# Kernel tuning notes

Hardware: AMD Instinct MI355X
Metric: run time of the kernel (lower is better)

Reference implementation:

```python
import jax, jax.numpy as jnp
from jax import lax
import numpy as np

SLOPE = 0.01   # torch nn.LeakyReLU default
EPS = 1e-5     # BN eps
DN = ('NCDHW', 'OIDHW', 'NCDHW')


def conv3d(x, w, pad):
    return lax.conv_general_dilated(x, w, (1, 1, 1), pad, dimension_numbers=DN)


def bn(x, g, b):
    # BatchNorm1d over all active points == per-channel stats over (N, D, H, W)
    m = jnp.mean(x, axis=(0, 2, 3, 4), keepdims=True)
    v = jnp.var(x, axis=(0, 2, 3, 4), keepdims=True)
    return (x - m) * lax.rsqrt(v + EPS) * g.reshape(1, -1, 1, 1, 1) + b.reshape(1, -1, 1, 1, 1)


def lrelu(x):
    return jnp.where(x >= 0, x, SLOPE * x)


def setup_inputs() -> dict:
    key = jax.random.key(0)
    ks = jax.random.split(key, 8)
    Cin, Cout = 128, 64
    x = jax.random.normal(ks[0], (1, Cin, 16, 48, 48), jnp.float32)      # coarse sparse grid (all-active)
    skip = jax.random.normal(ks[1], (1, Cout, 32, 96, 96), jnp.float32)  # fine skip grid
    s = lambda k, shape, fan: jax.random.normal(k, shape, jnp.float32) * np.float32(1.0 / np.sqrt(fan))
    w_trans = s(ks[2], (Cout, Cin, 3, 3, 3), Cin * 27)
    w_up = s(ks[3], (Cout, Cout, 3, 3, 3), Cout * 27)
    w1 = s(ks[4], (Cout, Cout, 1, 3, 3), Cout * 9)
    w2 = s(ks[5], (Cout, Cout, 3, 1, 3), Cout * 9)
    w3 = s(ks[6], (Cout, Cout, 3, 3, 3), Cout * 27)
    g = jnp.ones((Cout,), jnp.float32)
    b = jnp.zeros((Cout,), jnp.float32)
    return dict(x=x, skip=skip, w_trans=w_trans, g_t=g, b_t=b, w_up=w_up,
                w1=w1, g1=g, b1=b, w2=w2, g2=g, b2=b, w3=w3, g3=g, b3=b)


def reference(x, skip, w_trans, g_t, b_t, w_up, w1, g1, b1, w2, g2, b2, w3, g3, b3):
    # trans_conv (subm 3x3x3) -> LeakyReLU -> BN
    xt = bn(lrelu(conv3d(x, w_trans, [(1, 1)] * 3)), g_t, b_t)
    up = lax.conv_general_dilated(xt, w_up, (1, 1, 1), [(1, 2)] * 3,
                                  lhs_dilation=(2, 2, 2), dimension_numbers=DN)
    up = up + skip
    up = bn(lrelu(conv3d(up, w1, [(0, 0), (1, 1), (1, 1)])), g1, b1)  # conv1x3 (1,3,3)
    up = bn(lrelu(conv3d(up, w2, [(1, 1), (0, 0), (1, 1)])), g2, b2)  # conv3x1 (3,1,3)
    up = bn(lrelu(conv3d(up, w3, [(1, 1)] * 3)), g3, b3)              # conv3x3 (3,3,3)
    return up
```

## Files before the change

kernel.cpp:

```cpp
#include <hip/hip_runtime.h>

#define SLOPE 0.01f
#define BN_EPS 1e-5f

typedef __attribute__((ext_vector_type(8))) short short8;
typedef __attribute__((ext_vector_type(4))) float f32x4;

static constexpr int D1 = 32, H1 = 96, W1_ = 96;
static constexpr int HW1 = H1 * W1_, DHW1 = D1 * HW1;
static constexpr int D0 = 16, H0 = 48, W0 = 48;
static constexpr int HW0 = H0 * W0, DHW0 = D0 * HW0;

static constexpr int FP_PLPTS = 98 * 98;
static constexpr int CP_PLPTS = 50 * 50;
static constexpr int FP_ELEMS = 33 * FP_PLPTS * 64;

__device__ __forceinline__ short f2bf(float f) {
    unsigned u = __builtin_bit_cast(unsigned, f);
    unsigned r = (u + 0x7fffu + ((u >> 16) & 1u)) >> 16;
    return (short)r;
}
__device__ __forceinline__ float bf2f(short s) {
    unsigned u = ((unsigned)(unsigned short)s) << 16;
    return __builtin_bit_cast(float, u);
}
__device__ __forceinline__ int pidx_fine(int s) {
    int z = s / HW1; int r = s - z * HW1; int y = r / W1_; int x = r - y * W1_;
    return z * FP_PLPTS + (y + 1) * 98 + (x + 1);
}
__device__ __forceinline__ int pidx_coarse(int s) {
    int z = s / HW0; int r = s - z * HW0; int y = r / W0; int x = r - y * W0;
    return z * CP_PLPTS + (y + 1) * 50 + (x + 1);
}
__device__ __forceinline__ void gload16(const void* g, void* l) {
    __builtin_amdgcn_global_load_lds(
        (const __attribute__((address_space(1))) void*)g,
        (__attribute__((address_space(3))) void*)l, 16, 0, 0);
}

__global__ __launch_bounds__(256)
void to_cl_pad128(const float* __restrict__ in, short* __restrict__ out)
{
    __shared__ float t[64][65];
    const int s0 = blockIdx.x * 64, c0 = blockIdx.y * 64;
    const int tid = threadIdx.x;
    {
        const int cpr = tid >> 2, ch = tid & 3;
        const float4* ip = (const float4*)(in + (size_t)(c0 + cpr) * DHW0 + s0 + ch * 16);
        #pragma unroll
        for (int i = 0; i < 4; ++i) {
            float4 v = ip[i]; int sb = ch * 16 + i * 4;
            t[sb][cpr] = v.x; t[sb + 1][cpr] = v.y; t[sb + 2][cpr] = v.z; t[sb + 3][cpr] = v.w;
        }
    }
    __syncthreads();
    {
        const int spr = tid >> 2, cc = (tid & 3) * 16;
        short8 o0, o1;
        #pragma unroll
        for (int q = 0; q < 8; ++q) { o0[q] = f2bf(t[spr][cc + q]); o1[q] = f2bf(t[spr][cc + 8 + q]); }
        const int p = pidx_coarse(s0 + spr);
        short* op = out + (size_t)p * 128 + c0 + cc;
        *(short8*)op = o0;
        *(short8*)(op + 8) = o1;
    }
}

__global__ __launch_bounds__(256)
void to_cl_bf16(const float* __restrict__ in, short* __restrict__ out, int S)
{
    __shared__ float t[64][65];
    const int s0 = blockIdx.x * 64;
    const int tid = threadIdx.x;
    {
        const int cpr = tid >> 2, ch = tid & 3;
        const float4* ip = (const float4*)(in + (size_t)cpr * S + s0 + ch * 16);
        #pragma unroll
        for (int i = 0; i < 4; ++i) {
            float4 v = ip[i]; int sb = ch * 16 + i * 4;
            t[sb][cpr] = v.x; t[sb + 1][cpr] = v.y; t[sb + 2][cpr] = v.z; t[sb + 3][cpr] = v.w;
        }
    }
    __syncthreads();
    {
        const int spr = tid >> 2, cc = (tid & 3) * 16;
        short8 o0, o1;
        #pragma unroll
        for (int q = 0; q < 8; ++q) { o0[q] = f2bf(t[spr][cc + q]); o1[q] = f2bf(t[spr][cc + 8 + q]); }
        short* op = out + (size_t)(s0 + spr) * 64 + cc;
        *(short8*)op = o0;
        *(short8*)(op + 8) = o1;
    }
}

__device__ __forceinline__ void rp(const float* __restrict__ w, short* __restrict__ dst,
                                   int CIN, int KSZ, int i)
{
    int t = i / (64 * CIN); int r = i % (64 * CIN); int o = r / CIN; int ci = r % CIN;
    dst[i] = f2bf(w[(size_t)(o * CIN + ci) * KSZ + t]);
}
__global__ __launch_bounds__(256)
void prep_all(const float* __restrict__ wt, const float* __restrict__ wu,
              const float* __restrict__ w1, const float* __restrict__ w2,
              const float* __restrict__ w3, short* dt, short* du,
              short* d1, short* d2, short* d3)
{
    int i = blockIdx.x * 256 + threadIdx.x;
    if (i < 221184) { rp(wt, dt, 128, 27, i); return; } i -= 221184;
    if (i < 110592) { rp(wu, du, 64, 27, i); return; } i -= 110592;
    if (i < 36864)  { rp(w1, d1, 64, 9, i);  return; } i -= 36864;
    if (i < 36864)  { rp(w2, d2, 64, 9, i);  return; } i -= 36864;
    if (i < 110592) rp(w3, d3, 64, 27, i);
}

__global__ void finalize_stats(const float* __restrict__ stats, const float* __restrict__ g,
                               const float* __restrict__ b, float invN, float* __restrict__ aff)
{
    int c = threadIdx.x;
    float m = stats[c] * invN;
    float var = stats[64 + c] * invN - m * m;
    float rstd = rsqrtf(var + BN_EPS);
    float sc = g[c] * rstd;
    aff[c] = sc;
    aff[64 + c] = b[c] - m * sc;
}

template<int MODE>
__global__ __launch_bounds__(256)
void affine_pad(short* __restrict__ buf, const float* __restrict__ aff, int n8)
{
    int i = blockIdx.x * 256 + threadIdx.x;
    if (i >= n8) return;
    int s = i >> 3, cb = (i & 7) * 8;
    int p = (MODE == 1) ? pidx_fine(s) : pidx_coarse(s);
    short* ptr = buf + (size_t)p * 64 + cb;
    short8 v = *(const short8*)ptr;
    short8 o;
    #pragma unroll
    for (int q = 0; q < 8; ++q) {
        int c = cb + q;
        o[q] = f2bf(bf2f(v[q]) * aff[c] + aff[64 + c]);
    }
    *(short8*)ptr = o;
}

__global__ __launch_bounds__(256)
void final_out(const short* __restrict__ in, float* __restrict__ out, const float* __restrict__ aff)
{
    __shared__ float t[64][65];
    const int s0 = blockIdx.x * 64;
    const int tid = threadIdx.x;
    {
        const int spr = tid >> 2, ch = tid & 3;
        const short8* ip = (const short8*)(in + (size_t)(s0 + spr) * 64 + ch * 16);
        short8 v0 = ip[0], v1 = ip[1];
        #pragma unroll
        for (int q = 0; q < 8; ++q) { int c = ch * 16 + q;     t[spr][c] = bf2f(v0[q]) * aff[c] + aff[64 + c]; }
        #pragma unroll
        for (int q = 0; q < 8; ++q) { int c = ch * 16 + 8 + q; t[spr][c] = bf2f(v1[q]) * aff[c] + aff[64 + c]; }
    }
    __syncthreads();
    {
        const int c = tid >> 2, sc = (tid & 3) * 16;
        #pragma unroll
        for (int i = 0; i < 4; ++i) {
            float4 w;
            w.x = t[sc + 4 * i][c]; w.y = t[sc + 4 * i + 1][c];
            w.z = t[sc + 4 * i + 2][c]; w.w = t[sc + 4 * i + 3][c];
            *(float4*)(out + (size_t)c * DHW1 + s0 + sc + 4 * i) = w;
        }
    }
}

__global__ __launch_bounds__(256)
void zero_misc(short* __restrict__ PadA, short* __restrict__ PadB,
               short* __restrict__ X0, short* __restrict__ Y0, float* __restrict__ stats)
{
    const short8 z8 = {0, 0, 0, 0, 0, 0, 0, 0};
    int i = blockIdx.x * 256 + threadIdx.x;
    constexpr int T_F = 33 * 3104 + 76832;
    constexpr int T_X = 17 * 3136 + 40000;
    constexpr int T_Y = 17 * 1568 + 20000;
    constexpr int TOT = 2 * T_F + T_X + T_Y + 128;
    if (i >= TOT) return;

    auto fine_off = [](int q) -> size_t {
        if (q < 33 * 3104) {
            int pl = q / 3104, e = q % 3104, p = e >> 3, c = e & 7;
            int y, x;
            if (p < 98) { y = 0; x = p; }
            else if (p < 196) { y = 97; x = p - 98; }
            else { int q2 = p - 196; y = 1 + (q2 >> 1); x = (q2 & 1) ? 97 : 0; }
            return ((size_t)pl * FP_PLPTS + y * 98 + x) * 64 + c * 8;
        }
        int q2 = q - 33 * 3104;
        return (size_t)32 * FP_PLPTS * 64 + (size_t)q2 * 8;
    };
    auto co_off = [](int q, int CPR) -> size_t {
        const int EPP = 196 * CPR;
        if (q < 17 * EPP) {
            int pl = q / EPP, e = q % EPP, p = e / CPR, c = e % CPR;
            int y, x;
            if (p < 50) { y = 0; x = p; }
            else if (p < 100) { y = 49; x = p - 50; }
            else { int r = p - 100; y = 1 + (r >> 1); x = (r & 1) ? 49 : 0; }
            return ((size_t)pl * CP_PLPTS + y * 50 + x) * (CPR * 8) + c * 8;
        }
        int q2 = q - 17 * EPP;
        return (size_t)16 * CP_PLPTS * (CPR * 8) + (size_t)q2 * 8;
    };

    if (i < T_F) { *(short8*)(PadA + fine_off(i)) = z8; return; } i -= T_F;
    if (i < T_F) { *(short8*)(PadB + fine_off(i)) = z8; return; } i -= T_F;
    if (i < T_X) { *(short8*)(X0 + co_off(i, 16)) = z8; return; } i -= T_X;
    if (i < T_Y) { *(short8*)(Y0 + co_off(i, 8)) = z8; return; } i -= T_Y;
    float4 zf = {0.f, 0.f, 0.f, 0.f};
    *(float4*)((char*)stats + (size_t)i * 16) = zf;
}

template<int MG, int CIN, int KD, int KH, int KW, int PD, int PH, int PW,
         int GD, int GH, int GW, int OUTMODE, bool STATS>
__global__ __launch_bounds__(256, 2)
void convmm5(const short* __restrict__ A, const short* __restrict__ Wt,
             short* __restrict__ Out, float* __restrict__ stats)
{
    constexpr int MR   = 64 * MG;
    constexpr int KSZ  = KD * KH * KW;
    constexpr int PPW  = GW + 2;
    constexpr int PLP  = (GH + 2) * PPW;
    constexpr int HWg  = GH * GW;
    constexpr int CPR  = CIN / 8;
    constexpr int L2C  = (CIN == 64) ? 3 : 4;
    constexpr int RPI  = 64 / CPR;
    constexpr int ASZ  = MR * CIN * 2;
    constexpr int BSZ  = 64 * CIN * 2;
    constexpr int API  = ASZ / 4096;
    constexpr int BPI  = BSZ / 4096;
    constexpr int KCN  = CIN / 32;
    constexpr int S_IF = API + BPI;

    __shared__ char smem[2 * ASZ + 2 * BSZ];

    const int tid = threadIdx.x, lane = tid & 63, wave = tid >> 6;
    const int rl = lane & 15, kg = lane >> 4;

    const int nwg = gridDim.x;
    const int bid = blockIdx.x;
    const int bswz = (nwg & 7) ? bid : ((bid & 7) * (nwg >> 3) + (bid >> 3));
    const int row0 = bswz * MR;

    int zA[API], yxA[API], cofA[API];
    #pragma unroll
    for (int i = 0; i < API; ++i) {
        const int gi = wave * API + i;
        const int r = gi * RPI + (lane >> L2C);
        const int s = row0 + r;
        const int z = s / HWg; const int rm = s - z * HWg;
        const int y = rm / GW; const int x = rm - y * GW;
        zA[i] = z;
        yxA[i] = (y + 1) * PPW + (x + 1);
        cofA[i] = ((lane & (CPR - 1)) ^ (r & 7)) * 8;
    }
    int rB[BPI], cofB[BPI];
    #pragma unroll
    for (int i = 0; i < BPI; ++i) {
        const int gi = wave * BPI + i;
        const int r = gi * RPI + (lane >> L2C);
        rB[i] = r;
        cofB[i] = ((lane & (CPR - 1)) ^ (r & 7)) * 8;
    }

    auto stageA = [&](int bsel, int kd, int kh, int kw) {
        const int dyx = (kh - PH) * PPW + (kw - PW);
        #pragma unroll
        for (int i = 0; i < API; ++i) {
            int zp = zA[i] + (kd - PD);
            int pl = ((unsigned)zp < (unsigned)GD) ? zp : GD;
            const short* src = A + ((size_t)pl * PLP + yxA[i] + dyx) * CIN + cofA[i];
            void* dst = smem + bsel * ASZ + (wave * API + i) * 1024;
            gload16(src, dst);
        }
    };
    auto stageB = [&](int bsel, int t) {
        const short* wt = Wt + (size_t)t * 64 * CIN;
        #pragma unroll
        for (int i = 0; i < BPI; ++i) {
            const short* src = wt + rB[i] * CIN + cofB[i];
            void* dst = smem + 2 * ASZ + bsel * BSZ + (wave * BPI + i) * 1024;
            gload16(src, dst);
        }
    };

    f32x4 acc[MG][4];
    #pragma unroll
    for (int mg = 0; mg < MG; ++mg)
        #pragma unroll
        for (int ng = 0; ng < 4; ++ng)
            acc[mg][ng] = (f32x4){0.f, 0.f, 0.f, 0.f};

    auto comp = [&](int bsel) {
        const short* ab = (const short*)(smem + bsel * ASZ);
        const short* bb = (const short*)(smem + 2 * ASZ + bsel * BSZ);
        #pragma unroll
        for (int kc = 0; kc < KCN; ++kc) {
            short8 av[MG], bv[4];
            #pragma unroll
            for (int mg = 0; mg < MG; ++mg) {
                const int r = wave * (16 * MG) + mg * 16 + rl;
                const int c = (kc * 4 + kg) ^ (r & 7);
                av[mg] = *(const short8*)(ab + r * CIN + c * 8);
            }
            #pragma unroll
            for (int ng = 0; ng < 4; ++ng) {
                const int r = ng * 16 + rl;
                const int c = (kc * 4 + kg) ^ (r & 7);
                bv[ng] = *(const short8*)(bb + r * CIN + c * 8);
            }
            __builtin_amdgcn_s_setprio(1);
            #pragma unroll
            for (int mg = 0; mg < MG; ++mg)
                #pragma unroll
                for (int ng = 0; ng < 4; ++ng)
                    acc[mg][ng] = __builtin_amdgcn_mfma_f32_16x16x32_bf16(av[mg], bv[ng], acc[mg][ng], 0, 0, 0);
            __builtin_amdgcn_s_setprio(0);
        }
    };

    stageA(0, 0, 0, 0);
    stageB(0, 0);

    #pragma unroll
    for (int t = 0; t < KSZ; ++t) {
        const int cur = t & 1;
        if (t + 1 < KSZ) {
            const int t1 = t + 1;
            const int kd = t1 / (KH * KW), rm = t1 % (KH * KW);
            stageA(cur ^ 1, kd, rm / KW, rm % KW);
            stageB(cur ^ 1, t1);
            asm volatile("s_waitcnt vmcnt(%0)" :: "i"(S_IF) : "memory");
        } else {
            asm volatile("s_waitcnt vmcnt(0)" ::: "memory");
        }
        __builtin_amdgcn_s_barrier();
        __builtin_amdgcn_sched_barrier(0);
        comp(cur);
        asm volatile("s_waitcnt lgkmcnt(0)" ::: "memory");
        __builtin_amdgcn_sched_barrier(0);
        __builtin_amdgcn_s_barrier();
    }

    short (*tile)[64] = (short(*)[64])smem;
    float* red = (float*)(smem + 2 * ASZ);

    #pragma unroll
    for (int mg = 0; mg < MG; ++mg)
        #pragma unroll
        for (int ng = 0; ng < 4; ++ng)
            #pragma unroll
            for (int j = 0; j < 4; ++j) {
                float v = acc[mg][ng][j];
                if (STATS) v = (v >= 0.f) ? v : SLOPE * v;
                tile[wave * (16 * MG) + mg * 16 + kg * 4 + j][ng * 16 + rl] = f2bf(v);
            }
    __syncthreads();

    #pragma unroll
    for (int i = 0; i < MR / 32; ++i) {
        const int chunk = i * 256 + tid;
        const int r = chunk >> 3, cc = (chunk & 7) * 8;
        const int s = row0 + r;
        size_t o;
        if (OUTMODE == 0)      o = (size_t)s * 64 + cc;
        else if (OUTMODE == 1) o = (size_t)pidx_fine(s) * 64 + cc;
        else                   o = (size_t)pidx_coarse(s) * 64 + cc;
        *(short8*)(Out + o) = *(const short8*)&tile[r][cc];
    }

    if (STATS) {
        float s1 = 0.f, s2 = 0.f;
        const int col = tid & 63, rg = tid >> 6;
        #pragma unroll 4
        for (int r = rg * (MR / 4); r < (rg + 1) * (MR / 4); ++r) {
            float v = bf2f(tile[r][col]); s1 += v; s2 += v * v;
        }
        red[rg * 64 + col] = s1;
        red[256 + rg * 64 + col] = s2;
        __syncthreads();
        if (tid < 64) {
            float a = red[tid] + red[64 + tid] + red[128 + tid] + red[192 + tid];
            float b = red[256 + tid] + red[320 + tid] + red[384 + tid] + red[448 + tid];
            atomicAdd(&stats[tid], a);
            atomicAdd(&stats[64 + tid], b);
        }
    }
}

template<int KD, int KH, int PD, int PH, int OUTMODE, bool STATS>
__global__ __launch_bounds__(128, 1)
void convmm7(const short* __restrict__ A, const short* __restrict__ Wt,
             short* __restrict__ Out, float* __restrict__ stats)
{
    constexpr int KSZ = KD * KH * 3, NG = KD * KH;
    constexpr int PLP = FP_PLPTS;
    constexpr int ABYTES = 208 * 128;
    constexpr int BBYTES = 8192;
    __shared__ __align__(16) char smem[2 * ABYTES + 2 * BBYTES];

    const int tid = threadIdx.x, lane = tid & 63, wave = tid >> 6;
    const int rl = lane & 15, kg = lane >> 4;

    const int nwg = gridDim.x, bid = blockIdx.x;
    const int bswz = (bid & 7) * (nwg >> 3) + (bid >> 3);
    const int s0 = bswz * 192;
    const int z0 = s0 / HW1;
    const int y0 = (s0 - z0 * HW1) / 96;

    const int ptl = lane >> 3;
    const int csl = (lane & 7) ^ ptl;

    auto stageA = [&](int bsel, int g) {
        const int kd = g / KH, kh = g % KH;
        const int zp = z0 + kd - PD;
        const int pl = ((unsigned)zp < 32u) ? zp : 32;
        const int ys = y0 + kh - PH;
        const size_t base = (size_t)pl * PLP + (size_t)(ys + 1) * 98;
        #pragma unroll
        for (int i = 0; i < 13; ++i) {
            const int ii = wave * 13 + i;
            const short* src = A + (base + ii * 8 + ptl) * 64 + csl * 8;
            gload16(src, smem + bsel * ABYTES + ii * 1024);
        }
    };
    auto stageB = [&](int bsel, int t) {
        const short* wt = Wt + (size_t)t * 4096;
        #pragma unroll
        for (int i = 0; i < 4; ++i) {
            const int ii = wave * 4 + i;
            const short* src = wt + (ii * 8 + ptl) * 64 + csl * 8;
            gload16(src, smem + 2 * ABYTES + bsel * BBYTES + ii * 1024);
        }
    };

    f32x4 acc[6][4];
    #pragma unroll
    for (int mg = 0; mg < 6; ++mg)
        #pragma unroll
        for (int ng = 0; ng < 4; ++ng)
            acc[mg][ng] = (f32x4){0.f, 0.f, 0.f, 0.f};

    const int jb = wave * 98 + rl;

    stageA(0, 0);
    stageB(0, 0);

    #pragma unroll
    for (int t = 0; t < KSZ; ++t) {
        const int g = t / 3, kw = t % 3;
        if (kw == 0 && g + 1 < NG) stageA((g + 1) & 1, g + 1);
        if (t + 1 < KSZ) stageB((t + 1) & 1, t + 1);
        if (t == KSZ - 1)
            asm volatile("s_waitcnt vmcnt(0)" ::: "memory");
        else if (kw == 0 && g + 1 < NG)
            asm volatile("s_waitcnt vmcnt(17)" ::: "memory");
        else
            asm volatile("s_waitcnt vmcnt(4)" ::: "memory");
        __builtin_amdgcn_s_barrier();
        __builtin_amdgcn_sched_barrier(0);

        const char* ab = smem + (g & 1) * ABYTES;
        const char* bb = smem + 2 * ABYTES + (t & 1) * BBYTES;
        #pragma unroll
        for (int kc = 0; kc < 2; ++kc) {
            short8 bv[4], av[6];
            #pragma unroll
            for (int ng = 0; ng < 4; ++ng) {
                const int row = ng * 16 + rl;
                bv[ng] = *(const short8*)(bb + row * 128 + (((kc * 4 + kg) ^ (rl & 7)) << 4));
            }
            #pragma unroll
            for (int mg = 0; mg < 6; ++mg) {
                const int j = jb + mg * 16 + kw;
                av[mg] = *(const short8*)(ab + j * 128 + (((kc * 4 + kg) ^ (j & 7)) << 4));
            }
            __builtin_amdgcn_s_setprio(1);
            #pragma unroll
            for (int mg = 0; mg < 6; ++mg)
                #pragma unroll
                for (int ng = 0; ng < 4; ++ng)
                    acc[mg][ng] = __builtin_amdgcn_mfma_f32_16x16x32_bf16(av[mg], bv[ng], acc[mg][ng], 0, 0, 0);
            __builtin_amdgcn_s_setprio(0);
        }
        asm volatile("s_waitcnt lgkmcnt(0)" ::: "memory");
        __builtin_amdgcn_sched_barrier(0);
        __builtin_amdgcn_s_barrier();
    }

    short (*tile)[64] = (short(*)[64])smem;
    float* red = (float*)(smem + 192 * 64 * 2);

    #pragma unroll
    for (int mg = 0; mg < 6; ++mg)
        #pragma unroll
        for (int ng = 0; ng < 4; ++ng)
            #pragma unroll
            for (int j = 0; j < 4; ++j) {
                float v = acc[mg][ng][j];
                if (STATS) v = (v >= 0.f) ? v : SLOPE * v;
                tile[wave * 96 + mg * 16 + kg * 4 + j][ng * 16 + rl] = f2bf(v);
            }
    __syncthreads();

    #pragma unroll
    for (int i = 0; i < 12; ++i) {
        const int chunk = i * 128 + tid;
        const int r = chunk >> 3, cc = (chunk & 7) * 8;
        const int s = s0 + r;
        size_t o;
        if (OUTMODE == 0) o = (size_t)s * 64 + cc;
        else              o = (size_t)pidx_fine(s) * 64 + cc;
        *(short8*)(Out + o) = *(const short8*)&tile[r][cc];
    }

    if (STATS) {
        float s1 = 0.f, s2 = 0.f;
        const int col = tid & 63, rg = tid >> 6;
        #pragma unroll 4
        for (int r = rg * 96; r < rg * 96 + 96; ++r) {
            float v = bf2f(tile[r][col]); s1 += v; s2 += v * v;
        }
        red[rg * 64 + col] = s1;
        red[128 + rg * 64 + col] = s2;
        __syncthreads();
        if (tid < 64) {
            atomicAdd(&stats[tid], red[tid] + red[64 + tid]);
            atomicAdd(&stats[64 + tid], red[128 + tid] + red[192 + tid]);
        }
    }
}

__global__ __launch_bounds__(256, 2)
void tconv_cls(const short* __restrict__ Y, const short* __restrict__ Wt,
               const short* __restrict__ SK, short* __restrict__ Out)
{
    const int cls = blockIdx.y;
    const int pz = (cls >> 2) & 1, py = (cls >> 1) & 1, px = cls & 1;
    const int tid = threadIdx.x, lane = tid & 63, wave = tid >> 6;
    const int rl = lane & 15, kg = lane >> 4;
    const int row0 = blockIdx.x * 256;

    int zin0[4], zin1[4];
    #pragma unroll
    for (int mg = 0; mg < 4; ++mg) {
        int s = row0 + wave * 64 + mg * 16 + rl;
        int zc = s / HW0; int r = s - zc * HW0; int yc = r / W0; int xc = r - yc * W0;
        int ib = ((yc + 1) * 50 + (xc + 1)) * 64 + kg * 8;
        zin0[mg] = zc * (CP_PLPTS * 64) + ib;
        zin1[mg] = ((zc + 1 < 16) ? zc + 1 : 16) * (CP_PLPTS * 64) + ib;
    }
    const int boff = rl * 64 + kg * 8;

    f32x4 acc[4][4];
    #pragma unroll
    for (int mg = 0; mg < 4; ++mg)
        #pragma unroll
        for (int ng = 0; ng < 4; ++ng)
            acc[mg][ng] = (f32x4){0.f, 0.f, 0.f, 0.f};

    for (int a = 0; a <= pz; ++a) {
        const int kd = pz ? 2 * a : 1;
        for (int b = 0; b <= py; ++b) {
            const int kh = py ? 2 * b : 1;
            for (int c = 0; c <= px; ++c) {
                const int kw = px ? 2 * c : 1;
                const int t = kd * 9 + kh * 3 + kw;
                const int dlt = (b * 50 + c) * 64;
                int ao[4];
                #pragma unroll
                for (int mg = 0; mg < 4; ++mg)
                    ao[mg] = (a ? zin1[mg] : zin0[mg]) + dlt;
                #pragma unroll
                for (int kc = 0; kc < 2; ++kc) {
                    short8 av[4], bv[4];
                    #pragma unroll
                    for (int mg = 0; mg < 4; ++mg)
                        av[mg] = *(const short8*)(Y + ao[mg] + kc * 32);
                    #pragma unroll
                    for (int ng = 0; ng < 4; ++ng)
                        bv[ng] = *(const short8*)(Wt + (t * 64 + ng * 16) * 64 + boff + kc * 32);
                    #pragma unroll
                    for (int mg = 0; mg < 4; ++mg)
                        #pragma unroll
                        for (int ng = 0; ng < 4; ++ng)
                            acc[mg][ng] = __builtin_amdgcn_mfma_f32_16x16x32_bf16(av[mg], bv[ng], acc[mg][ng], 0, 0, 0);
                }
            }
        }
    }

    __shared__ short tile[256][72];
    #pragma unroll
    for (int mg = 0; mg < 4; ++mg)
        #pragma unroll
        for (int ng = 0; ng < 4; ++ng)
            #pragma unroll
            for (int j = 0; j < 4; ++j)
                tile[wave * 64 + mg * 16 + kg * 4 + j][ng * 16 + rl] = f2bf(acc[mg][ng][j]);
    __syncthreads();

    #pragma unroll
    for (int i = 0; i < 8; ++i) {
        int chunk = i * 256 + tid;
        int r = chunk >> 3, cc = (chunk & 7) * 8;
        int sl = row0 + r;
        int zc = sl / HW0; int rr = sl - zc * HW0; int yc = rr / W0; int xc = rr - yc * W0;
        int z = 2 * zc + pz, y = 2 * yc + py, x = 2 * xc + px;
        size_t so = (size_t)((z * H1 + y) * W1_ + x) * 64 + cc;
        size_t po = (size_t)(z * FP_PLPTS + (y + 1) * 98 + (x + 1)) * 64 + cc;
        short8 v = *(const short8*)&tile[r][cc];
        short8 skv = *(const short8*)(SK + so);
        short8 o;
        #pragma unroll
        for (int q = 0; q < 8; ++q) o[q] = f2bf(bf2f(v[q]) + bf2f(skv[q]));
        *(short8*)(Out + po) = o;
    }
}

extern "C" void kernel_launch(void* const* d_in, const int* in_sizes, int n_in,
                              void* d_out, int out_size, void* d_ws, size_t ws_size,
                              hipStream_t stream)
{
    const float* x       = (const float*)d_in[0];
    const float* skip    = (const float*)d_in[1];
    const float* w_trans = (const float*)d_in[2];
    const float* g_t     = (const float*)d_in[3];
    const float* b_t     = (const float*)d_in[4];
    const float* w_up    = (const float*)d_in[5];
    const float* w1      = (const float*)d_in[6];
    const float* g1      = (const float*)d_in[7];
    const float* b1      = (const float*)d_in[8];
    const float* w2      = (const float*)d_in[9];
    const float* g2      = (const float*)d_in[10];
    const float* b2      = (const float*)d_in[11];
    const float* w3      = (const float*)d_in[12];
    const float* g3      = (const float*)d_in[13];
    const float* b3      = (const float*)d_in[14];
    float* out = (float*)d_out;

    char* ws = (char*)d_ws;
    short* PadA = (short*)ws;
    short* PadB = (short*)(ws + (size_t)FP_ELEMS * 2);
    float* stats = (float*)(ws + (size_t)FP_ELEMS * 4);

    float* st0 = stats;       float* af0 = stats + 512;
    float* st1 = stats + 128; float* af1 = stats + 512 + 128;
    float* st2 = stats + 256; float* af2 = stats + 512 + 256;
    float* st3 = stats + 384; float* af3 = stats + 512 + 384;

    char* ob = (char*)d_out;
    short* X0  = (short*)ob;
    short* Y0  = (short*)(ob + 10880000);
    short* SKb = (short*)(ob + 16320000);
    short* wt_t  = (short*)(ob + 54068736);
    short* wt_up = wt_t + 221184;
    short* wt_1  = wt_up + 110592;
    short* wt_2  = wt_1 + 36864;
    short* wt_3  = wt_2 + 36864;

    zero_misc<<<(2 * (33 * 3104 + 76832) + (17 * 3136 + 40000) + (17 * 1568 + 20000) + 128 + 255) / 256,
               256, 0, stream>>>(PadA, PadB, X0, Y0, stats);

    prep_all<<<2016, 256, 0, stream>>>(w_trans, w_up, w1, w2, w3,
                                       wt_t, wt_up, wt_1, wt_2, wt_3);

    to_cl_pad128<<<dim3(DHW0 / 64, 2), 256, 0, stream>>>(x, X0);
    to_cl_bf16<<<DHW1 / 64, 256, 0, stream>>>(skip, SKb, DHW1);

    convmm5<1, 128, 3, 3, 3, 1, 1, 1, 16, 48, 48, 2, true>
        <<<DHW0 / 64, 256, 0, stream>>>(X0, wt_t, Y0, st0);
    finalize_stats<<<1, 64, 0, stream>>>(st0, g_t, b_t, 1.f / DHW0, af0);
    affine_pad<2><<<(DHW0 * 8 + 255) / 256, 256, 0, stream>>>(Y0, af0, DHW0 * 8);

    tconv_cls<<<dim3(DHW0 / 256, 8), 256, 0, stream>>>(Y0, wt_up, SKb, PadA);

    convmm7<1, 3, 0, 1, 1, true>
        <<<DHW1 / 192, 128, 0, stream>>>(PadA, wt_1, PadB, st1);
    finalize_stats<<<1, 64, 0, stream>>>(st1, g1, b1, 1.f / DHW1, af1);
    affine_pad<1><<<(DHW1 * 8 + 255) / 256, 256, 0, stream>>>(PadB, af1, DHW1 * 8);

    convmm7<3, 1, 1, 0, 1, true>
        <<<DHW1 / 192, 128, 0, stream>>>(PadB, wt_2, PadA, st2);
    finalize_stats<<<1, 64, 0, stream>>>(st2, g2, b2, 1.f / DHW1, af2);
    affine_pad<1><<<(DHW1 * 8 + 255) / 256, 256, 0, stream>>>(PadA, af2, DHW1 * 8);

    convmm7<3, 3, 1, 1, 0, true>
        <<<DHW1 / 192, 128, 0, stream>>>(PadA, wt_3, PadB, st3);
    finalize_stats<<<1, 64, 0, stream>>>(st3, g3, b3, 1.f / DHW1, af3);

    final_out<<<DHW1 / 64, 256, 0, stream>>>(PadB, out, af3);
}
```

Before: 410.2 us.

## Fold BatchNorm affine into next conv weights and bias, drop affine passes

Removes the separate affine_pad passes over the large activation buffers by folding each BN scale into the following conv's weights and its shift into a per-output bias. Halo cells are filled with -shift/scale so that padded positions still map to zero after the fold. The fine conv kernel also switches from staging B in LDS to loading weights straight into registers, with new waitcnt accounting. Risks include division by a near-zero scale, bf16 rounding of the halo value, and the per-class bias for the transposed conv.

```diff
diff --git a/kernel.cpp b/kernel.cpp
--- a/kernel.cpp
+++ b/kernel.cpp
@@ -93,24 +93,21 @@
     }
 }
 
-__device__ __forceinline__ void rp(const float* __restrict__ w, short* __restrict__ dst,
-                                   int CIN, int KSZ, int i)
-{
-    int t = i / (64 * CIN); int r = i % (64 * CIN); int o = r / CIN; int ci = r % CIN;
-    dst[i] = f2bf(w[(size_t)(o * CIN + ci) * KSZ + t]);
-}
 __global__ __launch_bounds__(256)
-void prep_all(const float* __restrict__ wt, const float* __restrict__ wu,
-              const float* __restrict__ w1, const float* __restrict__ w2,
-              const float* __restrict__ w3, short* dt, short* du,
-              short* d1, short* d2, short* d3)
+void prep_all(const float* __restrict__ wt, const float* __restrict__ w1,
+              short* dt, short* d1)
 {
     int i = blockIdx.x * 256 + threadIdx.x;
-    if (i < 221184) { rp(wt, dt, 128, 27, i); return; } i -= 221184;
-    if (i < 110592) { rp(wu, du, 64, 27, i); return; } i -= 110592;
-    if (i < 36864)  { rp(w1, d1, 64, 9, i);  return; } i -= 36864;
-    if (i < 36864)  { rp(w2, d2, 64, 9, i);  return; } i -= 36864;
-    if (i < 110592) rp(w3, d3, 64, 27, i);
+    if (i < 221184) {
+        int t = i / 8192; int r = i % 8192; int o = r >> 7; int ci = r & 127;
+        dt[i] = f2bf(wt[(size_t)(o * 128 + ci) * 27 + t]);
+        return;
+    }
+    i -= 221184;
+    if (i < 36864) {
+        int t = i / 4096; int r = i & 4095; int o = r >> 6; int ci = r & 63;
+        d1[i] = f2bf(w1[(size_t)(o * 64 + ci) * 9 + t]);
+    }
 }
 
 __global__ void finalize_stats(const float* __restrict__ stats, const float* __restrict__ g,
@@ -125,25 +122,6 @@
     aff[64 + c] = b[c] - m * sc;
 }
 
-template<int MODE>
-__global__ __launch_bounds__(256)
-void affine_pad(short* __restrict__ buf, const float* __restrict__ aff, int n8)
-{
-    int i = blockIdx.x * 256 + threadIdx.x;
-    if (i >= n8) return;
-    int s = i >> 3, cb = (i & 7) * 8;
-    int p = (MODE == 1) ? pidx_fine(s) : pidx_coarse(s);
-    short* ptr = buf + (size_t)p * 64 + cb;
-    short8 v = *(const short8*)ptr;
-    short8 o;
-    #pragma unroll
-    for (int q = 0; q < 8; ++q) {
-        int c = cb + q;
-        o[q] = f2bf(bf2f(v[q]) * aff[c] + aff[64 + c]);
-    }
-    *(short8*)ptr = o;
-}
-
 __global__ __launch_bounds__(256)
 void final_out(const short* __restrict__ in, float* __restrict__ out, const float* __restrict__ aff)
 {
@@ -181,7 +159,7 @@
     constexpr int T_F = 33 * 3104 + 76832;
     constexpr int T_X = 17 * 3136 + 40000;
     constexpr int T_Y = 17 * 1568 + 20000;
-    constexpr int TOT = 2 * T_F + T_X + T_Y + 128;
+    constexpr int TOT = 2 * T_F + T_X + T_Y + 432;
     if (i >= TOT) return;
 
     auto fine_off = [](int q) -> size_t {
@@ -216,6 +194,118 @@
     if (i < T_Y) { *(short8*)(Y0 + co_off(i, 8)) = z8; return; } i -= T_Y;
     float4 zf = {0.f, 0.f, 0.f, 0.f};
     *(float4*)((char*)stats + (size_t)i * 16) = zf;
+}
+
+template<int KSZ>
+__global__ __launch_bounds__(256)
+void prep_fine(const float* __restrict__ w, const float* __restrict__ aff,
+               short* __restrict__ dst, float* __restrict__ bias,
+               short* __restrict__ buf)
+{
+    __shared__ float red[256];
+    constexpr int NSC = KSZ * 4096 / 256;
+    int b = blockIdx.x;
+    if (b < NSC) {
+        int i = b * 256 + threadIdx.x;
+        int t = i / 4096; int r = i & 4095; int o = r >> 6; int ci = r & 63;
+        dst[i] = f2bf(w[(size_t)(o * 64 + ci) * KSZ + t] * aff[ci]);
+        return;
+    }
+    b -= NSC;
+    if (b < 64) {
+        int o = b;
+        float p = 0.f;
+        for (int i = threadIdx.x; i < 64 * KSZ; i += 256) {
+            int ci = i / KSZ, t = i % KSZ;
+            p += w[(size_t)(o * 64 + ci) * KSZ + t] * aff[64 + ci];
+        }
+        red[threadIdx.x] = p;
+        __syncthreads();
+        #pragma unroll
+        for (int off = 128; off > 0; off >>= 1) {
+            if (threadIdx.x < off) red[threadIdx.x] += red[threadIdx.x + off];
+            __syncthreads();
+        }
+        if (threadIdx.x == 0) bias[o] = red[0];
+        return;
+    }
+    b -= 64;
+    int q = b * 256 + threadIdx.x;
+    constexpr int T_F = 33 * 3104 + 76832;
+    if (q >= T_F) return;
+    size_t off; int cb;
+    if (q < 33 * 3104) {
+        int pl = q / 3104, e = q % 3104, p = e >> 3; cb = e & 7;
+        int y, x;
+        if (p < 98) { y = 0; x = p; }
+        else if (p < 196) { y = 97; x = p - 98; }
+        else { int r = p - 196; y = 1 + (r >> 1); x = (r & 1) ? 97 : 0; }
+        off = ((size_t)pl * FP_PLPTS + y * 98 + x) * 64 + cb * 8;
+    } else {
+        int q2 = q - 33 * 3104; cb = q2 & 7;
+        off = (size_t)32 * FP_PLPTS * 64 + (size_t)q2 * 8;
+    }
+    short8 hv;
+    #pragma unroll
+    for (int k = 0; k < 8; ++k) { int c = cb * 8 + k; hv[k] = f2bf(-aff[64 + c] / aff[c]); }
+    *(short8*)(buf + off) = hv;
+}
+
+__global__ __launch_bounds__(256)
+void prep_up(const float* __restrict__ wup, const float* __restrict__ aff,
+             short* __restrict__ dst, float* __restrict__ bias_up,
+             short* __restrict__ Y0)
+{
+    __shared__ float red[64];
+    int b = blockIdx.x;
+    if (b < 432) {
+        int i = b * 256 + threadIdx.x;
+        int t = i / 4096; int r = i & 4095; int o = r >> 6; int ci = r & 63;
+        dst[i] = f2bf(wup[(size_t)(o * 64 + ci) * 27 + t] * aff[ci]);
+        return;
+    }
+    b -= 432;
+    if (b < 512) {
+        int cls = b >> 6, o = b & 63;
+        int pz = (cls >> 2) & 1, py = (cls >> 1) & 1, px = cls & 1;
+        int ci = threadIdx.x;
+        if (ci < 64) {
+            float p = 0.f;
+            for (int a = 0; a <= pz; ++a) { int kd = pz ? 2 * a : 1;
+                for (int b2 = 0; b2 <= py; ++b2) { int kh = py ? 2 * b2 : 1;
+                    for (int c2 = 0; c2 <= px; ++c2) { int kw = px ? 2 * c2 : 1;
+                        p += wup[(size_t)(o * 64 + ci) * 27 + kd * 9 + kh * 3 + kw];
+                    } } }
+            red[ci] = p * aff[64 + ci];
+        }
+        __syncthreads();
+        if (threadIdx.x == 0) {
+            float s = 0.f;
+            for (int k = 0; k < 64; ++k) s += red[k];
+            bias_up[cls * 64 + o] = s;
+        }
+        return;
+    }
+    b -= 512;
+    int q = b * 256 + threadIdx.x;
+    constexpr int T_Y = 17 * 1568 + 20000;
+    if (q >= T_Y) return;
+    size_t off; int cb;
+    if (q < 17 * 1568) {
+        int pl = q / 1568, e = q % 1568, p = e >> 3; cb = e & 7;
+        int y, x;
+        if (p < 50) { y = 0; x = p; }
+        else if (p < 100) { y = 49; x = p - 50; }
+        else { int r = p - 100; y = 1 + (r >> 1); x = (r & 1) ? 49 : 0; }
+        off = ((size_t)pl * CP_PLPTS + y * 50 + x) * 64 + cb * 8;
+    } else {
+        int q2 = q - 17 * 1568; cb = q2 & 7;
+        off = (size_t)16 * CP_PLPTS * 64 + (size_t)q2 * 8;
+    }
+    short8 hv;
+    #pragma unroll
+    for (int k = 0; k < 8; ++k) { int c = cb * 8 + k; hv[k] = f2bf(-aff[64 + c] / aff[c]); }
+    *(short8*)(Y0 + off) = hv;
 }
 
 template<int MG, int CIN, int KD, int KH, int KW, int PD, int PH, int PW,
@@ -395,16 +485,16 @@
     }
 }
 
-template<int KD, int KH, int PD, int PH, int OUTMODE, bool STATS>
+template<int KD, int KH, int PD, int PH, int OUTMODE>
 __global__ __launch_bounds__(128, 1)
-void convmm7(const short* __restrict__ A, const short* __restrict__ Wt,
+void convmm8(const short* __restrict__ A, const short* __restrict__ Wt,
+             const float* __restrict__ bias,
              short* __restrict__ Out, float* __restrict__ stats)
 {
-    constexpr int KSZ = KD * KH * 3, NG = KD * KH;
+    constexpr int NG = KD * KH, KSZ = NG * 3;
     constexpr int PLP = FP_PLPTS;
     constexpr int ABYTES = 208 * 128;
-    constexpr int BBYTES = 8192;
-    __shared__ __align__(16) char smem[2 * ABYTES + 2 * BBYTES];
+    __shared__ __align__(16) char smem[2 * ABYTES];
 
     const int tid = threadIdx.x, lane = tid & 63, wave = tid >> 6;
     const int rl = lane & 15, kg = lane >> 4;
@@ -431,52 +521,31 @@
             gload16(src, smem + bsel * ABYTES + ii * 1024);
         }
     };
-    auto stageB = [&](int bsel, int t) {
+    auto loadB = [&](short8 (&dst)[8], int t) {
         const short* wt = Wt + (size_t)t * 4096;
         #pragma unroll
-        for (int i = 0; i < 4; ++i) {
-            const int ii = wave * 4 + i;
-            const short* src = wt + (ii * 8 + ptl) * 64 + csl * 8;
-            gload16(src, smem + 2 * ABYTES + bsel * BBYTES + ii * 1024);
-        }
+        for (int kc = 0; kc < 2; ++kc)
+            #pragma unroll
+            for (int ng = 0; ng < 4; ++ng)
+                dst[kc * 4 + ng] = *(const short8*)(wt + (ng * 16 + rl) * 64 + (kc * 4 + kg) * 8);
     };
 
+    float bc[4];
+    #pragma unroll
+    for (int ng = 0; ng < 4; ++ng) bc[ng] = bias[ng * 16 + rl];
     f32x4 acc[6][4];
     #pragma unroll
     for (int mg = 0; mg < 6; ++mg)
         #pragma unroll
         for (int ng = 0; ng < 4; ++ng)
-            acc[mg][ng] = (f32x4){0.f, 0.f, 0.f, 0.f};
+            acc[mg][ng] = (f32x4){bc[ng], bc[ng], bc[ng], bc[ng]};
 
     const int jb = wave * 98 + rl;
 
-    stageA(0, 0);
-    stageB(0, 0);
-
-    #pragma unroll
-    for (int t = 0; t < KSZ; ++t) {
-        const int g = t / 3, kw = t % 3;
-        if (kw == 0 && g + 1 < NG) stageA((g + 1) & 1, g + 1);
-        if (t + 1 < KSZ) stageB((t + 1) & 1, t + 1);
-        if (t == KSZ - 1)
-            asm volatile("s_waitcnt vmcnt(0)" ::: "memory");
-        else if (kw == 0 && g + 1 < NG)
-            asm volatile("s_waitcnt vmcnt(17)" ::: "memory");
-        else
-            asm volatile("s_waitcnt vmcnt(4)" ::: "memory");
-        __builtin_amdgcn_s_barrier();
-        __builtin_amdgcn_sched_barrier(0);
-
-        const char* ab = smem + (g & 1) * ABYTES;
-        const char* bb = smem + 2 * ABYTES + (t & 1) * BBYTES;
+    auto compTap = [&](const short8 (&bv)[8], const char* ab, int kw) {
         #pragma unroll
         for (int kc = 0; kc < 2; ++kc) {
-            short8 bv[4], av[6];
-            #pragma unroll
-            for (int ng = 0; ng < 4; ++ng) {
-                const int row = ng * 16 + rl;
-                bv[ng] = *(const short8*)(bb + row * 128 + (((kc * 4 + kg) ^ (rl & 7)) << 4));
-            }
+            short8 av[6];
             #pragma unroll
             for (int mg = 0; mg < 6; ++mg) {
                 const int j = jb + mg * 16 + kw;
@@ -487,8 +556,32 @@
             for (int mg = 0; mg < 6; ++mg)
                 #pragma unroll
                 for (int ng = 0; ng < 4; ++ng)
-                    acc[mg][ng] = __builtin_amdgcn_mfma_f32_16x16x32_bf16(av[mg], bv[ng], acc[mg][ng], 0, 0, 0);
+                    acc[mg][ng] = __builtin_amdgcn_mfma_f32_16x16x32_bf16(av[mg], bv[kc * 4 + ng], acc[mg][ng], 0, 0, 0);
             __builtin_amdgcn_s_setprio(0);
+        }
+    };
+
+    short8 brA[8], brB[8];
+    stageA(0, 0);
+    loadB(brA, 0);
+
+    #pragma unroll
+    for (int g = 0; g < NG; ++g) {
+        if (g + 1 < NG) stageA((g + 1) & 1, g + 1);
+        #pragma unroll
+        for (int kw = 0; kw < 3; ++kw) {
+            const int t = 3 * g + kw;
+            if (t + 1 < KSZ) {
+                if ((t + 1) & 1) loadB(brB, t + 1); else loadB(brA, t + 1);
+            }
+            const bool moreA = (g + 1 < NG), moreB = (t + 1 < KSZ);
+            if (moreA && moreB)      asm volatile("s_waitcnt vmcnt(21)" ::: "memory");
+            else if (moreB)          asm volatile("s_waitcnt vmcnt(8)" ::: "memory");
+            else                     asm volatile("s_waitcnt vmcnt(0)" ::: "memory");
+            if (kw == 0) __builtin_amdgcn_s_barrier();
+            __builtin_amdgcn_sched_barrier(0);
+            const char* ab = smem + (g & 1) * ABYTES;
+            if (t & 1) compTap(brB, ab, kw); else compTap(brA, ab, kw);
         }
         asm volatile("s_waitcnt lgkmcnt(0)" ::: "memory");
         __builtin_amdgcn_sched_barrier(0);
@@ -505,7 +598,7 @@
             #pragma unroll
             for (int j = 0; j < 4; ++j) {
                 float v = acc[mg][ng][j];
-                if (STATS) v = (v >= 0.f) ? v : SLOPE * v;
+                v = (v >= 0.f) ? v : SLOPE * v;
                 tile[wave * 96 + mg * 16 + kg * 4 + j][ng * 16 + rl] = f2bf(v);
             }
     __syncthreads();
@@ -521,7 +614,7 @@
         *(short8*)(Out + o) = *(const short8*)&tile[r][cc];
     }
 
-    if (STATS) {
+    {
         float s1 = 0.f, s2 = 0.f;
         const int col = tid & 63, rg = tid >> 6;
         #pragma unroll 4
@@ -540,6 +633,7 @@
 
 __global__ __launch_bounds__(256, 2)
 void tconv_cls(const short* __restrict__ Y, const short* __restrict__ Wt,
+               const float* __restrict__ bias_up,
                const short* __restrict__ SK, short* __restrict__ Out)
 {
     const int cls = blockIdx.y;
@@ -559,12 +653,15 @@
     }
     const int boff = rl * 64 + kg * 8;
 
+    float bc[4];
+    #pragma unroll
+    for (int ng = 0; ng < 4; ++ng) bc[ng] = bias_up[cls * 64 + ng * 16 + rl];
     f32x4 acc[4][4];
     #pragma unroll
     for (int mg = 0; mg < 4; ++mg)
         #pragma unroll
         for (int ng = 0; ng < 4; ++ng)
-            acc[mg][ng] = (f32x4){0.f, 0.f, 0.f, 0.f};
+            acc[mg][ng] = (f32x4){bc[ng], bc[ng], bc[ng], bc[ng]};
 
     for (int a = 0; a <= pz; ++a) {
         const int kd = pz ? 2 * a : 1;
@@ -655,6 +752,10 @@
     float* st1 = stats + 128; float* af1 = stats + 512 + 128;
     float* st2 = stats + 256; float* af2 = stats + 512 + 256;
     float* st3 = stats + 384; float* af3 = stats + 512 + 384;
+    float* bias2 = stats + 1024;
+    float* bias3 = stats + 1088;
+    float* bias_up = stats + 1152;
+    float* bias_z  = stats + 1664;
 
     char* ob = (char*)d_out;
     short* X0  = (short*)ob;
@@ -666,11 +767,12 @@
     short* wt_2  = wt_1 + 36864;
     short* wt_3  = wt_2 + 36864;
 
-    zero_misc<<<(2 * (33 * 3104 + 76832) + (17 * 3136 + 40000) + (17 * 1568 + 20000) + 128 + 255) / 256,
-               256, 0, stream>>>(PadA, PadB, X0, Y0, stats);
-
-    prep_all<<<2016, 256, 0, stream>>>(w_trans, w_up, w1, w2, w3,
-                                       wt_t, wt_up, wt_1, wt_2, wt_3);
+    constexpr int T_F = 33 * 3104 + 76832;
+    constexpr int T_X = 17 * 3136 + 40000;
+    constexpr int T_Y = 17 * 1568 + 20000;
+    zero_misc<<<(2 * T_F + T_X + T_Y + 432 + 255) / 256, 256, 0, stream>>>(PadA, PadB, X0, Y0, stats);
+
+    prep_all<<<(221184 + 36864 + 255) / 256, 256, 0, stream>>>(w_trans, w1, wt_t, wt_1);
 
     to_cl_pad128<<<dim3(DHW0 / 64, 2), 256, 0, stream>>>(x, X0);
     to_cl_bf16<<<DHW1 / 64, 256, 0, stream>>>(skip, SKb, DHW1);
@@ -678,22 +780,22 @@
     convmm5<1, 128, 3, 3, 3, 1, 1, 1, 16, 48, 48, 2, true>
         <<<DHW0 / 64, 256, 0, stream>>>(X0, wt_t, Y0, st0);
     finalize_stats<<<1, 64, 0, stream>>>(st0, g_t, b_t, 1.f / DHW0, af0);
-    affine_pad<2><<<(DHW0 * 8 + 255) / 256, 256, 0, stream>>>(Y0, af0, DHW0 * 8);
-
-    tconv_cls<<<dim3(DHW0 / 256, 8), 256, 0, stream>>>(Y0, wt_up, SKb, PadA);
-
-    convmm7<1, 3, 0, 1, 1, true>
-        <<<DHW1 / 192, 128, 0, stream>>>(PadA, wt_1, PadB, st1);
+    prep_up<<<432 + 512 + (T_Y + 255) / 256, 256, 0, stream>>>(w_up, af0, wt_up, bias_up, Y0);
+
+    tconv_cls<<<dim3(DHW0 / 256, 8), 256, 0, stream>>>(Y0, wt_up, bias_up, SKb, PadA);
+
+    convmm8<1, 3, 0, 1, 1>
+        <<<DHW1 / 192, 128, 0, stream>>>(PadA, wt_1, bias_z, PadB, st1);
     finalize_stats<<<1, 64, 0, stream>>>(st1, g1, b1, 1.f / DHW1, af1);
-    affine_pad<1><<<(DHW1 * 8 + 255) / 256, 256, 0, stream>>>(PadB, af1, DHW1 * 8);
-
-    convmm7<3, 1, 1, 0, 1, true>
-        <<<DHW1 / 192, 128, 0, stream>>>(PadB, wt_2, PadA, st2);
+    prep_fine<9><<<144 + 64 + (T_F + 255) / 256, 256, 0, stream>>>(w2, af1, wt_2, bias2, PadB);
+
+    convmm8<3, 1, 1, 0, 1>
+        <<<DHW1 / 192, 128, 0, stream>>>(PadB, wt_2, bias2, PadA, st2);
     finalize_stats<<<1, 64, 0, stream>>>(st2, g2, b2, 1.f / DHW1, af2);
-    affine_pad<1><<<(DHW1 * 8 + 255) / 256, 256, 0, stream>>>(PadA, af2, DHW1 * 8);
-
-    convmm7<3, 3, 1, 1, 0, true>
-        <<<DHW1 / 192, 128, 0, stream>>>(PadA, wt_3, PadB, st3);
+    prep_fine<27><<<432 + 64 + (T_F + 255) / 256, 256, 0, stream>>>(w3, af2, wt_3, bias3, PadA);
+
+    convmm8<3, 3, 1, 1, 0>
+        <<<DHW1 / 192, 128, 0, stream>>>(PadA, wt_3, bias3, PadB, st3);
     finalize_stats<<<1, 64, 0, stream>>>(st3, g3, b3, 1.f / DHW1, af3);
 
     final_out<<<DHW1 / 64, 256, 0, stream>>>(PadB, out, af3);
```

Measured after the change: 444.5 us. +8.4%, slower.
